# Kernel tuning notes

Measured on AMD Instinct MI355X. Metric: run time of the kernel, lower is better.

## Reference

```python
import jax, jax.numpy as jnp
import numpy as np

SEQ_LEN, BATCH, INPUT_SIZE = 2048, 16, 1024
HIDDEN_SIZE = 1024  # must equal INPUT_SIZE (source uses input[t] as highway residual)
NUM_MATRICES = 3


def setup_inputs() -> dict:
    key = jax.random.key(0)
    k_in, k_w, k_b, k_v = jax.random.split(key, 4)
    val_range = (3.0 / INPUT_SIZE) ** 0.5
    inp = {
        "input": jax.random.normal(k_in, (SEQ_LEN, BATCH, INPUT_SIZE), dtype=jnp.float32),
        "weight": jax.random.uniform(k_w, (INPUT_SIZE, HIDDEN_SIZE * NUM_MATRICES),
                                     minval=-val_range, maxval=val_range, dtype=jnp.float32),
        # reset_parameters zeroes bias/v; use small random values so the gating is non-trivial
        "bias": jax.random.normal(k_b, (2 * HIDDEN_SIZE,), dtype=jnp.float32) * 0.1,
        "v": jax.random.normal(k_v, (2 * HIDDEN_SIZE,), dtype=jnp.float32) * 0.1,
    }
    return inp


def reference(input, weight, bias, v):
    seq_len, batch, input_size = input.shape
    hidden = HIDDEN_SIZE
    # One big matmul up-front: [S,B,I] @ [I,3H] -> [S,B,H,3]
    U = (input @ weight).reshape(seq_len, batch, hidden, NUM_MATRICES)
    U0, U1, U2 = U[..., 0], U[..., 1], U[..., 2]
    b0, b1 = bias.reshape(2, hidden)
    # Source quirk: v0, v1 are (erroneously) taken from bias, not v. Preserve it.
    v0, v1 = bias.reshape(2, hidden)

    c0 = jnp.zeros((batch, hidden), dtype=input.dtype)

    def step(c_prev, xs):
        u0, u1, u2, x_t = xs
        f_t = jax.nn.sigmoid(u0 + v0 * c_prev + b0)
        r_t = jax.nn.sigmoid(u1 + v1 * c_prev + b1)
        c_t = f_t * c_prev + (1.0 - f_t) * u2
        h_t = r_t * c_t + (1.0 - r_t) * x_t
        return c_t, (h_t, c_t)

    _, (H, C) = jax.lax.scan(step, c0, (U0, U1, U2, input))
    return H, C
```

## Files before the change

kernel.cpp:

```cpp
#include <hip/hip_runtime.h>
#include <hip/hip_bf16.h>
#include <stdint.h>
#include <stddef.h>

#define SEQ 2048
#define BATCH 16
#define HID 1024
#define MM (SEQ*BATCH)
#define NN (3*HID)
#define KK HID

typedef __bf16 bf16x8 __attribute__((ext_vector_type(8)));
typedef float floatx4 __attribute__((ext_vector_type(4)));

template <typename UT> __device__ inline void storeU(UT* p, float v);
template <> __device__ inline void storeU<float>(float* p, float v) { *p = v; }
template <> __device__ inline void storeU<__bf16>(__bf16* p, float v) { *p = (__bf16)v; }
template <typename UT> __device__ inline float loadU(const UT* p);
template <> __device__ inline float loadU<float>(const float* p) { return *p; }
template <> __device__ inline float loadU<__bf16>(const __bf16* p) { return (float)*p; }

__global__ __launch_bounds__(256) void cast_a_kernel(const float* __restrict__ in,
                                                     __bf16* __restrict__ out) {
  size_t i = (size_t)blockIdx.x * 256 + threadIdx.x;
  float4 v = ((const float4*)in)[i];
  typedef __bf16 bf16x4 __attribute__((ext_vector_type(4)));
  bf16x4 o;
  o[0] = (__bf16)v.x; o[1] = (__bf16)v.y; o[2] = (__bf16)v.z; o[3] = (__bf16)v.w;
  ((bf16x4*)out)[i] = o;
}

__global__ __launch_bounds__(256) void pack_w_kernel(const float* __restrict__ w,
                                                     __bf16* __restrict__ wp) {
  __shared__ float tile[32][33];
  int n0 = blockIdx.x * 32, k0 = blockIdx.y * 32;
  int tx = threadIdx.x, ty = threadIdx.y;
#pragma unroll
  for (int r = 0; r < 4; r++)
    tile[ty + 8*r][tx] = w[(size_t)(k0 + ty + 8*r) * NN + n0 + tx];
  __syncthreads();
#pragma unroll
  for (int r = 0; r < 4; r++)
    wp[(size_t)(n0 + ty + 8*r) * KK + k0 + tx] = (__bf16)tile[tx][ty + 8*r];
}

template <typename UT>
__global__ __launch_bounds__(256) void gemm_kernel(const __bf16* __restrict__ A,
                                                   const __bf16* __restrict__ B,
                                                   UT* __restrict__ U) {
  __shared__ __align__(16) char smem[32768];
  const int tid  = threadIdx.x;
  const int lane = tid & 63;
  const int wave = tid >> 6;

  const int bid = blockIdx.y * (NN / 128) + blockIdx.x;
  const int nid = (bid & 7) * ((MM / 128) * (NN / 128) / 8) + (bid >> 3);
  const int tileN = (nid % (NN / 128)) * 128;
  const int tileM = (nid / (NN / 128)) * 128;

  const char* gsrc[8];
  uint32_t    ldsoff[8];
#pragma unroll
  for (int j = 0; j < 8; j++) {
    int s   = j * 256 + tid;
    int isB = s >> 10;
    int s2  = s & 1023;
    int row = s2 >> 3;
    int cs  = s2 & 7;
    int kc  = cs ^ (row & 7);
    const __bf16* base = isB ? (B + (size_t)(tileN + row) * KK)
                             : (A + (size_t)(tileM + row) * KK);
    gsrc[j]   = (const char*)(base + kc * 8);
    ldsoff[j] = (uint32_t)(j * 4096 + wave * 1024);
  }

  const int wm = (wave >> 1) * 64;
  const int wn = (wave & 1) * 64;
  const int g  = lane >> 4;

  uint32_t aoff[4], boff[4];
#pragma unroll
  for (int i = 0; i < 4; i++) {
    int row  = wm + i * 16 + (lane & 15);
    aoff[i]  = (uint32_t)((row * 8 + (g ^ (row & 7))) * 16);
    int nrow = wn + i * 16 + (lane & 15);
    boff[i]  = (uint32_t)(16384 + (nrow * 8 + (g ^ (nrow & 7))) * 16);
  }

  floatx4 acc[4][4];
#pragma unroll
  for (int mi = 0; mi < 4; mi++)
#pragma unroll
    for (int ni = 0; ni < 4; ni++) acc[mi][ni] = (floatx4)0.0f;

  for (int it = 0; it < KK / 64; ++it) {
    __syncthreads();
#pragma unroll
    for (int j = 0; j < 8; j++)
      __builtin_amdgcn_global_load_lds(
          (const __attribute__((address_space(1))) void*)(gsrc[j]),
          (__attribute__((address_space(3))) void*)(smem + ldsoff[j]), 16, 0, 0);
#pragma unroll
    for (int j = 0; j < 8; j++) gsrc[j] += 128;
    __syncthreads();

#pragma unroll
    for (int ks = 0; ks < 2; ++ks) {
      bf16x8 a[4], b[4];
#pragma unroll
      for (int i = 0; i < 4; i++) {
        a[i] = *(const bf16x8*)(smem + (aoff[i] ^ (ks * 64)));
        b[i] = *(const bf16x8*)(smem + (boff[i] ^ (ks * 64)));
      }
#pragma unroll
      for (int mi = 0; mi < 4; mi++)
#pragma unroll
        for (int ni = 0; ni < 4; ni++)
          acc[mi][ni] = __builtin_amdgcn_mfma_f32_16x16x32_bf16(
              a[mi], b[ni], acc[mi][ni], 0, 0, 0);
    }
  }

  const int r0 = (lane >> 4) * 4;
  const int cc = lane & 15;
#pragma unroll
  for (int mi = 0; mi < 4; mi++)
#pragma unroll
    for (int ni = 0; ni < 4; ni++) {
      int col = tileN + wn + ni * 16 + cc;
#pragma unroll
      for (int r = 0; r < 4; r++) {
        int row = tileM + wm + mi * 16 + r0 + r;
        storeU(&U[(size_t)row * NN + col], acc[mi][ni][r]);
      }
    }
}

__device__ inline float sigmoidf_fast(float z) {
  return __builtin_amdgcn_rcpf(1.0f + __expf(-z));
}

#define SCH 32

__global__ __launch_bounds__(256) void scan_pc_kernel(const float* __restrict__ U,
                                                      const float* __restrict__ x,
                                                      const float* __restrict__ bias,
                                                      float* __restrict__ out) {
  __shared__ __align__(16) char smem[2 * SCH * 1024];
  const int tid  = threadIdx.x;
  const int wave = tid >> 6;
  const int lane = tid & 63;
  const int b    = blockIdx.x >> 4;
  const int h0   = (blockIdx.x & 15) * 64;

  const char* const ub = (const char*)(U + (size_t)b * NN + 3 * h0);
  const char* const xb = (const char*)(x + (size_t)b * HID + h0);

  float b0 = 0.f, b1 = 0.f, c = 0.f;
  if (wave == 0) { b0 = bias[h0 + lane]; b1 = bias[HID + h0 + lane]; }

  auto issue = [&](int ci) {
    char* dst = smem + (ci & 1) * (SCH * 1024);
    for (int s = wave - 1; s < SCH; s += 3) {
      size_t t = (size_t)ci * SCH + s;
      const char* us = ub + t * (size_t)(BATCH * NN * 4);
      const char* xs = xb + t * (size_t)(BATCH * HID * 4);
      const char* src = (lane < 48) ? (us + lane * 16) : (xs + (lane - 48) * 16);
      __builtin_amdgcn_global_load_lds(
          (const __attribute__((address_space(1))) void*)src,
          (__attribute__((address_space(3))) void*)(dst + s * 1024), 16, 0, 0);
    }
  };

  if (wave > 0) issue(0);
  __syncthreads();

  for (int ci = 0; ci < SEQ / SCH; ++ci) {
    if (wave > 0) {
      if (ci + 1 < SEQ / SCH) issue(ci + 1);
    } else {
      const float* buf = (const float*)(smem + (ci & 1) * (SCH * 1024));
#pragma unroll 4
      for (int s = 0; s < SCH; ++s) {
        const float* p = buf + s * 256;
        float u0 = p[3 * lane];
        float u1 = p[3 * lane + 1];
        float u2 = p[3 * lane + 2];
        float xv = p[192 + lane];
        float f = sigmoidf_fast(u0 + b0 * c + b0);
        float r = sigmoidf_fast(u1 + b1 * c + b1);
        c = f * c + (1.0f - f) * u2;
        float ht = r * c + (1.0f - r) * xv;
        size_t o = (size_t)(ci * SCH + s) * (BATCH * HID) + (b * HID + h0 + lane);
        out[o] = ht;
        out[(size_t)SEQ * BATCH * HID + o] = c;
      }
    }
    __syncthreads();
  }
}

template <typename UT>
__global__ __launch_bounds__(64) void scan_kernel(const UT* __restrict__ U,
                                                  const float* __restrict__ x,
                                                  const float* __restrict__ bias,
                                                  float* __restrict__ out) {
  int idx = blockIdx.x * 64 + threadIdx.x;
  int b = idx >> 10, h = idx & 1023;
  float b0 = bias[h], b1 = bias[HID + h];

  const UT*    up = U + (size_t)b * NN + 3 * h;
  const float* xp = x + idx;
  float* Hout = out + idx;
  float* Cout = out + (size_t)SEQ * BATCH * HID + idx;

  constexpr int P = 16;
  float pu0[P], pu1[P], pu2[P], px[P];
#pragma unroll
  for (int i = 0; i < P; i++) {
    const UT* u = up + (size_t)i * (BATCH * NN);
    pu0[i] = loadU(u); pu1[i] = loadU(u + 1); pu2[i] = loadU(u + 2);
    px[i]  = xp[(size_t)i * (BATCH * HID)];
  }

  float c = 0.0f;
  int tt = 0;
  for (; tt < SEQ - P; tt += P) {
#pragma unroll
    for (int i = 0; i < P; i++) {
      int t = tt + i;
      float u0 = pu0[i], u1 = pu1[i], u2 = pu2[i], xv = px[i];
      const UT* u = up + (size_t)(t + P) * (BATCH * NN);
      pu0[i] = loadU(u); pu1[i] = loadU(u + 1); pu2[i] = loadU(u + 2);
      px[i]  = xp[(size_t)(t + P) * (BATCH * HID)];

      float f = sigmoidf_fast(u0 + b0 * c + b0);
      float r = sigmoidf_fast(u1 + b1 * c + b1);
      c = f * c + (1.0f - f) * u2;
      float ht = r * c + (1.0f - r) * xv;
      Cout[(size_t)t * (BATCH * HID)] = c;
      Hout[(size_t)t * (BATCH * HID)] = ht;
    }
  }
#pragma unroll
  for (int i = 0; i < P; i++) {
    int t = tt + i;
    float f = sigmoidf_fast(pu0[i] + b0 * c + b0);
    float r = sigmoidf_fast(pu1[i] + b1 * c + b1);
    c = f * c + (1.0f - f) * pu2[i];
    float ht = r * c + (1.0f - r) * px[i];
    Cout[(size_t)t * (BATCH * HID)] = c;
    Hout[(size_t)t * (BATCH * HID)] = ht;
  }
}

extern "C" void kernel_launch(void* const* d_in, const int* in_sizes, int n_in,
                              void* d_out, int out_size, void* d_ws, size_t ws_size,
                              hipStream_t stream) {
  const float* input  = (const float*)d_in[0];
  const float* weight = (const float*)d_in[1];
  const float* bias   = (const float*)d_in[2];
  float* out = (float*)d_out;

  char* ws = (char*)d_ws;
  const size_t apB = (size_t)MM * KK * 2;
  const size_t wpB = (size_t)NN * KK * 2;
  const size_t uF  = (size_t)MM * NN * 4;
  bool useF32 = ws_size >= uF + apB + wpB;
  size_t uB = useF32 ? uF : uF / 2;

  void*   Uv = (void*)ws;
  __bf16* Ap = (__bf16*)(ws + uB);
  __bf16* Wp = (__bf16*)(ws + uB + apB);

  cast_a_kernel<<<(MM * KK) / 4 / 256, 256, 0, stream>>>(input, Ap);
  pack_w_kernel<<<dim3(NN / 32, KK / 32), dim3(32, 8), 0, stream>>>(weight, Wp);

  if (useF32) {
    gemm_kernel<float><<<dim3(NN / 128, MM / 128), 256, 0, stream>>>(Ap, Wp, (float*)Uv);
    scan_pc_kernel<<<BATCH * 16, 256, 0, stream>>>((const float*)Uv, input, bias, out);
  } else {
    gemm_kernel<__bf16><<<dim3(NN / 128, MM / 128), 256, 0, stream>>>(Ap, Wp, (__bf16*)Uv);
    scan_kernel<__bf16><<<(BATCH * HID) / 64, 64, 0, stream>>>((const __bf16*)Uv, input, bias, out);
  }
}
```

Measured before the change: 788.8 us.

## Deepen scan prefetch to a four-slot ring and drop GEMM tile swizzle

The scan kernel's LDS double buffer becomes a four-slot ring, so producer waves keep up to three chunks of global-to-LDS loads in flight. Explicit partial vmcnt waits and raw s_barrier replace __syncthreads, which would drain all outstanding loads each iteration. The GEMM drops its grouped block-index remap and uses a plain row/column tile mapping, which may worsen L2 reuse. Quadrupling the scan kernel's LDS use may lower occupancy, and the hand-counted vmcnt values must match the number of loads each wave issues.

```diff
diff --git a/kernel.cpp b/kernel.cpp
--- a/kernel.cpp
+++ b/kernel.cpp
@@ -52,11 +52,8 @@
   const int tid  = threadIdx.x;
   const int lane = tid & 63;
   const int wave = tid >> 6;
-
-  const int bid = blockIdx.y * (NN / 128) + blockIdx.x;
-  const int nid = (bid & 7) * ((MM / 128) * (NN / 128) / 8) + (bid >> 3);
-  const int tileN = (nid % (NN / 128)) * 128;
-  const int tileM = (nid / (NN / 128)) * 128;
+  const int tileN = blockIdx.x * 128;
+  const int tileM = blockIdx.y * 128;
 
   const char* gsrc[8];
   uint32_t    ldsoff[8];
@@ -141,12 +138,14 @@
 }
 
 #define SCH 32
+#define RING 4
+#define NCH (SEQ / SCH)
 
 __global__ __launch_bounds__(256) void scan_pc_kernel(const float* __restrict__ U,
                                                       const float* __restrict__ x,
                                                       const float* __restrict__ bias,
                                                       float* __restrict__ out) {
-  __shared__ __align__(16) char smem[2 * SCH * 1024];
+  __shared__ __align__(16) char smem[RING * SCH * 1024];
   const int tid  = threadIdx.x;
   const int wave = tid >> 6;
   const int lane = tid & 63;
@@ -160,7 +159,7 @@
   if (wave == 0) { b0 = bias[h0 + lane]; b1 = bias[HID + h0 + lane]; }
 
   auto issue = [&](int ci) {
-    char* dst = smem + (ci & 1) * (SCH * 1024);
+    char* dst = smem + (ci & (RING - 1)) * (SCH * 1024);
     for (int s = wave - 1; s < SCH; s += 3) {
       size_t t = (size_t)ci * SCH + s;
       const char* us = ub + t * (size_t)(BATCH * NN * 4);
@@ -172,14 +171,26 @@
     }
   };
 
-  if (wave > 0) issue(0);
-  __syncthreads();
-
-  for (int ci = 0; ci < SEQ / SCH; ++ci) {
+  if (wave > 0) {
+    issue(0); issue(1); issue(2);
+    asm volatile("s_waitcnt vmcnt(20)" ::: "memory");
+  }
+  asm volatile("" ::: "memory");
+  __builtin_amdgcn_s_barrier();
+  asm volatile("" ::: "memory");
+
+  for (int ci = 0; ci < NCH; ++ci) {
     if (wave > 0) {
-      if (ci + 1 < SEQ / SCH) issue(ci + 1);
+      if (ci + 3 < NCH) {
+        issue(ci + 3);
+        asm volatile("s_waitcnt vmcnt(20)" ::: "memory");
+      } else if (ci + 2 < NCH) {
+        asm volatile("s_waitcnt vmcnt(10)" ::: "memory");
+      } else if (ci + 1 < NCH) {
+        asm volatile("s_waitcnt vmcnt(0)" ::: "memory");
+      }
     } else {
-      const float* buf = (const float*)(smem + (ci & 1) * (SCH * 1024));
+      const float* buf = (const float*)(smem + (ci & (RING - 1)) * (SCH * 1024));
 #pragma unroll 4
       for (int s = 0; s < SCH; ++s) {
         const float* p = buf + s * 256;
@@ -196,7 +207,9 @@
         out[(size_t)SEQ * BATCH * HID + o] = c;
       }
     }
-    __syncthreads();
+    asm volatile("" ::: "memory");
+    __builtin_amdgcn_s_barrier();
+    asm volatile("" ::: "memory");
   }
 }
 
```

After: 783.8 us. About the same (-0.6%).
